# Kernel tuning notes

Measured on AMD Instinct MI355X. Metric: run time of the kernel, lower is better.

Reference implementation:

```python
import jax, jax.numpy as jnp
import numpy as np

N = 100000   # nodes
E = 1000000  # edges (avg degree 10)
F_IN, H1, H2, C = 128, 64, 64, 16


def setup_inputs() -> dict:
    key = jax.random.key(0)
    ks = jax.random.split(key, 10)
    x = jax.random.normal(ks[0], (N, F_IN), dtype=jnp.float32)
    edge_src = jax.random.randint(ks[1], (E,), 0, N, dtype=jnp.int32)
    edge_dst = jax.random.randint(ks[2], (E,), 0, N, dtype=jnp.int32)
    # normalized-adjacency-like positive edge weights (~1/deg scale)
    edge_val = jax.random.uniform(ks[3], (E,), dtype=jnp.float32) * 0.1
    def glorot(k, fan_in, fan_out):
        s = np.float32(1.0 / np.sqrt(fan_in))
        return jax.random.normal(k, (fan_in, fan_out), dtype=jnp.float32) * s
    W1 = glorot(ks[4], F_IN, H1)
    W2 = glorot(ks[5], H1, H2)
    W3 = glorot(ks[6], H2, C)
    b1 = jnp.zeros((H1,), jnp.float32)
    b2 = jnp.zeros((H2,), jnp.float32)
    b3 = jnp.zeros((C,), jnp.float32)
    return {"x": x, "edge_val": edge_val, "W1": W1, "b1": b1,
            "W2": W2, "b2": b2, "W3": W3, "b3": b3,
            "edge_src": edge_src, "edge_dst": edge_dst}


def gcn_layer(h, W, b, edge_src, edge_dst, edge_val):
    # support = h @ W ; out = spmm(adj, support) + b
    support = h @ W                                  # [N, d_out]
    msg = support[edge_src] * edge_val[:, None]      # [E, d_out] gather + scale
    agg = jax.ops.segment_sum(msg, edge_dst, num_segments=N)  # scatter-add
    return agg + b


def reference(x, edge_val, W1, b1, W2, b2, W3, b3, edge_src, edge_dst):
    # eval mode: F.dropout(training=False) is identity
    h = jax.nn.relu(gcn_layer(x, W1, b1, edge_src, edge_dst, edge_val))
    h = jax.nn.relu(gcn_layer(h, W2, b2, edge_src, edge_dst, edge_val))
    return gcn_layer(h, W3, b3, edge_src, edge_dst, edge_val)  # [N, C] logits
```

## Files before the change

### kernel.cpp

```cpp
#include <hip/hip_runtime.h>
#include <stdint.h>

#define N_NODES 100000
#define N_EDGES 1000000
#define NBUCK 98

typedef __attribute__((ext_vector_type(8))) __bf16 bf16x8;
typedef __attribute__((ext_vector_type(4))) float f32x4;

static __device__ __forceinline__ float bf2f(unsigned short u) {
    return __uint_as_float(((unsigned int)u) << 16);
}
static __device__ __forceinline__ unsigned short f2bf(float f) {
    unsigned int u = __float_as_uint(f);
    unsigned int r = (u + 0x7FFFu + ((u >> 16) & 1u)) >> 16;
    return (unsigned short)r;
}
static __device__ __forceinline__ float4 ld4_half(const unsigned short* p) {
    ushort4 u = *(const ushort4*)p;
    return make_float4(bf2f(u.x), bf2f(u.y), bf2f(u.z), bf2f(u.w));
}
static __device__ __forceinline__ void st4_half(unsigned short* p, float4 f) {
    ushort4 u;
    u.x = f2bf(f.x); u.y = f2bf(f.y); u.z = f2bf(f.z); u.w = f2bf(f.w);
    *(ushort4*)p = u;
}

static __device__ __forceinline__ float ldf(const void* p, size_t i, int bf) {
    return bf ? bf2f(((const unsigned short*)p)[i]) : ((const float*)p)[i];
}
static __device__ __forceinline__ float4 ldf4(const void* p, size_t i, int bf) {
    if (bf) return ld4_half((const unsigned short*)p + i);
    return *(const float4*)((const float*)p + i);
}

__global__ __launch_bounds__(256) void detect_kernel(const unsigned short* __restrict__ xs,
                                                     int* __restrict__ flag) {
    __shared__ int sz;
    if (threadIdx.x == 0) sz = 0;
    __syncthreads();
    int z = 0;
    for (int i = threadIdx.x; i < 1024; i += 256) {
        float av = fabsf(bf2f(xs[2 * i]));
        if (!(av <= 1048576.0f) || (av != 0.0f && av < 9.5367431640625e-07f)) z++;
    }
    atomicAdd(&sz, z);
    __syncthreads();
    if (threadIdx.x == 0) *flag = (sz > 256) ? 0 : 1;
}

__global__ __launch_bounds__(256) void bhist_kernel(const int* __restrict__ dst,
                                                    int* __restrict__ bcount) {
    __shared__ int cnt[NBUCK];
    int tid = threadIdx.x;
    for (int i = tid; i < NBUCK; i += 256) cnt[i] = 0;
    __syncthreads();
    int e0 = blockIdx.x * 4096;
#pragma unroll
    for (int i = 0; i < 16; ++i) {
        int e = e0 + i * 256 + tid;
        if (e < N_EDGES) atomicAdd(&cnt[dst[e] >> 10], 1);
    }
    __syncthreads();
    for (int i = tid; i < NBUCK; i += 256) {
        int c = cnt[i];
        if (c) atomicAdd(&bcount[i], c);
    }
}

__global__ __launch_bounds__(128) void bscan_kernel(const int* __restrict__ bcount,
                                                    int* __restrict__ bstart,
                                                    int* __restrict__ bcursor) {
    __shared__ int sh[128];
    int tid = threadIdx.x;
    int v = (tid < NBUCK) ? bcount[tid] : 0;
    sh[tid] = v;
    __syncthreads();
    for (int off = 1; off < 128; off <<= 1) {
        int t = 0;
        if (tid >= off) t = sh[tid - off];
        __syncthreads();
        if (tid >= off) sh[tid] += t;
        __syncthreads();
    }
    if (tid < NBUCK) {
        int excl = sh[tid] - v;
        bstart[tid] = excl;
        bcursor[tid] = excl;
    }
    if (tid == NBUCK - 1) bstart[NBUCK] = sh[tid];
}

__global__ __launch_bounds__(256) void part_kernel(const int* __restrict__ src,
                                                   const int* __restrict__ dst,
                                                   const void* __restrict__ val,
                                                   int* __restrict__ bcursor,
                                                   int2* __restrict__ part,
                                                   const int* __restrict__ flagp) {
    __shared__ int cnt[NBUCK];
    __shared__ int base[NBUCK];
    const int bf = *flagp;
    const int tid = threadIdx.x;
    const int e0 = blockIdx.x * 2048;
    for (int i = tid; i < NBUCK; i += 256) cnt[i] = 0;
    __syncthreads();
    int rank[8], bkt[8], pk[8], vb[8];
#pragma unroll
    for (int i = 0; i < 8; ++i) {
        int e = e0 + i * 256 + tid;
        bkt[i] = -1;
        if (e < N_EDGES) {
            int d = dst[e];
            int b = d >> 10;
            bkt[i] = b;
            pk[i] = src[e] | ((d & 1023) << 17);
            vb[i] = __float_as_int(ldf(val, e, bf));
            rank[i] = atomicAdd(&cnt[b], 1);
        }
    }
    __syncthreads();
    for (int i = tid; i < NBUCK; i += 256) {
        int c = cnt[i];
        base[i] = c ? atomicAdd(&bcursor[i], c) : 0;
    }
    __syncthreads();
#pragma unroll
    for (int i = 0; i < 8; ++i) {
        if (bkt[i] >= 0) part[(size_t)base[bkt[i]] + rank[i]] = make_int2(pk[i], vb[i]);
    }
}

__global__ __launch_bounds__(512) void place_kernel(const int* __restrict__ bstart,
                                                    const int2* __restrict__ part,
                                                    int* __restrict__ row_start,
                                                    int2* __restrict__ csr_rec) {
    __shared__ int cnt[1024];
    __shared__ int sums[512];
    const int tid = threadIdx.x;
    const int b = blockIdx.x;
    const int row0 = b << 10;
    const int nrows = min(1024, N_NODES - row0);
    const int s = bstart[b], e = bstart[b + 1];

    for (int i = tid; i < 1024; i += 512) cnt[i] = 0;
    __syncthreads();
    for (int j = s + tid; j < e; j += 512) {
        unsigned p = (unsigned)part[j].x;
        atomicAdd(&cnt[p >> 17], 1);
    }
    __syncthreads();
    int a0 = cnt[2 * tid], a1 = cnt[2 * tid + 1];
    int ts = a0 + a1;
    sums[tid] = ts;
    __syncthreads();
    for (int off = 1; off < 512; off <<= 1) {
        int t = 0;
        if (tid >= off) t = sums[tid - off];
        __syncthreads();
        if (tid >= off) sums[tid] += t;
        __syncthreads();
    }
    int excl = sums[tid] - ts;
    cnt[2 * tid] = s + excl;
    cnt[2 * tid + 1] = s + excl + a0;
    if (2 * tid < nrows)     row_start[row0 + 2 * tid] = s + excl;
    if (2 * tid + 1 < nrows) row_start[row0 + 2 * tid + 1] = s + excl + a0;
    if (b == NBUCK - 1 && tid == 0) row_start[N_NODES] = e;
    __syncthreads();
    for (int j = s + tid; j < e; j += 512) {
        int2 r = part[j];
        unsigned p = (unsigned)r.x;
        int pos = atomicAdd(&cnt[p >> 17], 1);
        csr_rec[pos] = make_int2((int)(p & 0x1FFFFu), r.y);
    }
}

template <int K, int M, bool DYNIN>
__global__ __launch_bounds__(256, 4) void mgemm_kernel(const void* __restrict__ hv_,
                                                       const void* __restrict__ W,
                                                       unsigned short* __restrict__ out,
                                                       const int* __restrict__ flagp) {
    constexpr int KP = K + 8;
    constexpr int NC = M / 16;
    constexpr int NK = K / 32;
    constexpr int NT = (N_NODES + 63) / 64;

    __shared__ unsigned short wt[M][KP];

    const int bf = *flagp;
    const int tid = threadIdx.x;

    for (int i = tid; i < K * M; i += 256) {
        int k = i / M, m = i % M;
        wt[m][k] = f2bf(ldf(W, i, bf));
    }
    __syncthreads();

    const int lane = tid & 63;
    const int qd = lane >> 4;
    const int ln = lane & 15;
    const int wrow = (tid >> 6) * 16;

    bf16x8 bfrag[NK][NC];
#pragma unroll
    for (int ks = 0; ks < NK; ++ks)
#pragma unroll
        for (int c = 0; c < NC; ++c)
            bfrag[ks][c] = *(const bf16x8*)&wt[c * 16 + ln][ks * 32 + qd * 8];

    for (int tile = blockIdx.x; tile < NT; tile += gridDim.x) {
        const int row = tile * 64 + wrow + ln;
        const bool ok = row < N_NODES;

        f32x4 acc[NC];
#pragma unroll
        for (int c = 0; c < NC; ++c) acc[c] = (f32x4){0.f, 0.f, 0.f, 0.f};

#pragma unroll
        for (int ks = 0; ks < NK; ++ks) {
            bf16x8 a;
            if (ok) {
                const size_t base = (size_t)row * K + ks * 32 + qd * 8;
                if (DYNIN && !bf) {
                    const float* xp = (const float*)hv_ + base;
                    float4 f0 = *(const float4*)xp;
                    float4 f1 = *(const float4*)(xp + 4);
                    ushort4 u0, u1;
                    u0.x = f2bf(f0.x); u0.y = f2bf(f0.y); u0.z = f2bf(f0.z); u0.w = f2bf(f0.w);
                    u1.x = f2bf(f1.x); u1.y = f2bf(f1.y); u1.z = f2bf(f1.z); u1.w = f2bf(f1.w);
                    ushort4 uu[2] = {u0, u1};
                    a = *(const bf16x8*)uu;
                } else {
                    a = *(const bf16x8*)((const unsigned short*)hv_ + base);
                }
            } else {
                a = (bf16x8)(__bf16)0.0f;
            }
#pragma unroll
            for (int c = 0; c < NC; ++c)
                acc[c] = __builtin_amdgcn_mfma_f32_16x16x32_bf16(a, bfrag[ks][c], acc[c], 0, 0, 0);
        }

#pragma unroll
        for (int c = 0; c < NC; ++c) {
#pragma unroll
            for (int r = 0; r < 4; ++r) {
                int orow = tile * 64 + wrow + qd * 4 + r;
                if (orow < N_NODES) out[(size_t)orow * M + c * 16 + ln] = f2bf(acc[c][r]);
            }
        }
    }
}

template <int M, bool RELU, bool DYNOUT>
__global__ __launch_bounds__(256) void spmm_kernel(const unsigned short* __restrict__ support,
                                                   const int* __restrict__ row_start,
                                                   const int2* __restrict__ csr_rec,
                                                   const void* __restrict__ bias,
                                                   void* __restrict__ out_,
                                                   const int* __restrict__ flagp) {
    constexpr int GROUP = M / 4;
    constexpr int GPB = 256 / GROUP;
    int bf = *flagp;
    int tid = threadIdx.x;
    int gid = blockIdx.x * GPB + tid / GROUP;
    int c0 = (tid % GROUP) * 4;
    if (gid >= N_NODES) return;
    int s = row_start[gid];
    int e = row_start[gid + 1];
    float a0 = ldf(bias, c0 + 0, bf);
    float a1 = ldf(bias, c0 + 1, bf);
    float a2 = ldf(bias, c0 + 2, bf);
    float a3 = ldf(bias, c0 + 3, bf);
    const unsigned short* supc = support + c0;

    int j = s;
    for (; j + 3 < e; j += 4) {
        int2 r0 = csr_rec[j + 0];
        int2 r1 = csr_rec[j + 1];
        int2 r2 = csr_rec[j + 2];
        int2 r3 = csr_rec[j + 3];
        float4 s0 = ld4_half(supc + (size_t)r0.x * M);
        float4 s1 = ld4_half(supc + (size_t)r1.x * M);
        float4 s2 = ld4_half(supc + (size_t)r2.x * M);
        float4 s3 = ld4_half(supc + (size_t)r3.x * M);
        float v0 = __int_as_float(r0.y);
        float v1 = __int_as_float(r1.y);
        float v2 = __int_as_float(r2.y);
        float v3 = __int_as_float(r3.y);
        a0 += v0 * s0.x; a1 += v0 * s0.y; a2 += v0 * s0.z; a3 += v0 * s0.w;
        a0 += v1 * s1.x; a1 += v1 * s1.y; a2 += v1 * s1.z; a3 += v1 * s1.w;
        a0 += v2 * s2.x; a1 += v2 * s2.y; a2 += v2 * s2.z; a3 += v2 * s2.w;
        a0 += v3 * s3.x; a1 += v3 * s3.y; a2 += v3 * s3.z; a3 += v3 * s3.w;
    }
    for (; j < e; ++j) {
        int2 rec = csr_rec[j];
        float v = __int_as_float(rec.y);
        float4 sp = ld4_half(supc + (size_t)rec.x * M);
        a0 += v * sp.x; a1 += v * sp.y; a2 += v * sp.z; a3 += v * sp.w;
    }
    if (RELU) {
        a0 = fmaxf(a0, 0.f); a1 = fmaxf(a1, 0.f);
        a2 = fmaxf(a2, 0.f); a3 = fmaxf(a3, 0.f);
    }
    float4 f = make_float4(a0, a1, a2, a3);
    if (DYNOUT) {
        if (bf) st4_half((unsigned short*)out_ + (size_t)gid * M + c0, f);
        else    *(float4*)((float*)out_ + (size_t)gid * M + c0) = f;
    } else {
        st4_half((unsigned short*)out_ + (size_t)gid * M + c0, f);
    }
}

extern "C" void kernel_launch(void* const* d_in, const int* in_sizes, int n_in,
                              void* d_out, int out_size, void* d_ws, size_t ws_size,
                              hipStream_t stream) {
    (void)in_sizes; (void)n_in; (void)out_size; (void)ws_size;
    const void* x  = d_in[0];
    const void* ev = d_in[1];
    const void* W1 = d_in[2];
    const void* b1 = d_in[3];
    const void* W2 = d_in[4];
    const void* b2 = d_in[5];
    const void* W3 = d_in[6];
    const void* b3 = d_in[7];
    const int* esrc = (const int*)d_in[8];
    const int* edst = (const int*)d_in[9];

    char* ws = (char*)d_ws;
    size_t off = 0;
    auto alloc = [&](size_t bytes) -> void* {
        void* p = ws + off;
        off = (off + bytes + 255) & ~(size_t)255;
        return p;
    };
    unsigned short* A = (unsigned short*)alloc((size_t)N_NODES * 64 * 2);
    unsigned short* B = (unsigned short*)alloc((size_t)N_NODES * 64 * 2);
    int* row_start  = (int*)alloc((size_t)(N_NODES + 1) * 4);
    int* bcount     = (int*)alloc(512);
    int* bstart     = (int*)alloc(512);
    int* bcursor    = (int*)alloc(512);
    int2* csr_rec   = (int2*)alloc((size_t)N_EDGES * 8);
    int* flagp      = (int*)alloc(256);
    int2* part      = (int2*)A;

    detect_kernel<<<1, 256, 0, stream>>>((const unsigned short*)x, flagp);

    hipMemsetAsync(bcount, 0, 512, stream);
    bhist_kernel<<<(N_EDGES + 4095) / 4096, 256, 0, stream>>>(edst, bcount);
    bscan_kernel<<<1, 128, 0, stream>>>(bcount, bstart, bcursor);
    part_kernel<<<(N_EDGES + 2047) / 2048, 256, 0, stream>>>(esrc, edst, ev, bcursor, part, flagp);
    place_kernel<<<NBUCK, 512, 0, stream>>>(bstart, part, row_start, csr_rec);

    int gm   = 1024;
    int gs64 = (N_NODES + 15) / 16;
    int g64  = (N_NODES + 63) / 64;

    mgemm_kernel<128, 64, true><<<gm, 256, 0, stream>>>(x, W1, A, flagp);
    spmm_kernel<64, true, false><<<gs64, 256, 0, stream>>>(A, row_start, csr_rec, b1, B, flagp);
    mgemm_kernel<64, 64, false><<<gm, 256, 0, stream>>>(B, W2, A, flagp);
    spmm_kernel<64, true, false><<<gs64, 256, 0, stream>>>(A, row_start, csr_rec, b2, B, flagp);
    mgemm_kernel<64, 16, false><<<gm, 256, 0, stream>>>(B, W3, A, flagp);
    spmm_kernel<16, false, true><<<g64, 256, 0, stream>>>(A, row_start, csr_rec, b3, d_out, flagp);
}
```

Measured before the change: 277.3 us.

## Fuse SpMM aggregation with following GEMM via shared-memory tile

The 64-wide SpMM+ReLU of layers 1 and 2 is merged with the next layer's dense matmul: each block gathers a 64-row tile into LDS as bf16, then runs MFMA against the next weight matrix. This drops two kernel launches and a round trip of the intermediate activations through global memory. The gather loop is also unrolled to 8 edges to keep more loads in flight. The first GEMM now reads weight fragments from LDS inside the loop instead of keeping them in registers. The fused kernel uses a persistent grid of 1024 blocks with barriers per tile, so fewer concurrent row gathers may hide less latency than the old per-row spmm grid.

```diff
diff --git a/kernel.cpp b/kernel.cpp
--- a/kernel.cpp
+++ b/kernel.cpp
@@ -175,6 +175,46 @@
     }
 }
 
+static __device__ __forceinline__ void row_gather(const unsigned short* __restrict__ supc,
+                                                  const int2* __restrict__ csr_rec,
+                                                  int s, int e, int M,
+                                                  float& a0, float& a1, float& a2, float& a3) {
+    int j = s;
+    for (; j + 7 < e; j += 8) {
+        int2 r[8];
+#pragma unroll
+        for (int t = 0; t < 8; ++t) r[t] = csr_rec[j + t];
+        float4 sp[8];
+#pragma unroll
+        for (int t = 0; t < 8; ++t) sp[t] = ld4_half(supc + (size_t)r[t].x * M);
+#pragma unroll
+        for (int t = 0; t < 8; ++t) {
+            float v = __int_as_float(r[t].y);
+            a0 += v * sp[t].x; a1 += v * sp[t].y; a2 += v * sp[t].z; a3 += v * sp[t].w;
+        }
+    }
+    if (j + 3 < e) {
+        int2 r[4];
+#pragma unroll
+        for (int t = 0; t < 4; ++t) r[t] = csr_rec[j + t];
+        float4 sp[4];
+#pragma unroll
+        for (int t = 0; t < 4; ++t) sp[t] = ld4_half(supc + (size_t)r[t].x * M);
+#pragma unroll
+        for (int t = 0; t < 4; ++t) {
+            float v = __int_as_float(r[t].y);
+            a0 += v * sp[t].x; a1 += v * sp[t].y; a2 += v * sp[t].z; a3 += v * sp[t].w;
+        }
+        j += 4;
+    }
+    for (; j < e; ++j) {
+        int2 rec = csr_rec[j];
+        float v = __int_as_float(rec.y);
+        float4 sp = ld4_half(supc + (size_t)rec.x * M);
+        a0 += v * sp.x; a1 += v * sp.y; a2 += v * sp.z; a3 += v * sp.w;
+    }
+}
+
 template <int K, int M, bool DYNIN>
 __global__ __launch_bounds__(256, 4) void mgemm_kernel(const void* __restrict__ hv_,
                                                        const void* __restrict__ W,
@@ -201,13 +241,6 @@
     const int ln = lane & 15;
     const int wrow = (tid >> 6) * 16;
 
-    bf16x8 bfrag[NK][NC];
-#pragma unroll
-    for (int ks = 0; ks < NK; ++ks)
-#pragma unroll
-        for (int c = 0; c < NC; ++c)
-            bfrag[ks][c] = *(const bf16x8*)&wt[c * 16 + ln][ks * 32 + qd * 8];
-
     for (int tile = blockIdx.x; tile < NT; tile += gridDim.x) {
         const int row = tile * 64 + wrow + ln;
         const bool ok = row < N_NODES;
@@ -225,10 +258,9 @@
                     const float* xp = (const float*)hv_ + base;
                     float4 f0 = *(const float4*)xp;
                     float4 f1 = *(const float4*)(xp + 4);
-                    ushort4 u0, u1;
-                    u0.x = f2bf(f0.x); u0.y = f2bf(f0.y); u0.z = f2bf(f0.z); u0.w = f2bf(f0.w);
-                    u1.x = f2bf(f1.x); u1.y = f2bf(f1.y); u1.z = f2bf(f1.z); u1.w = f2bf(f1.w);
-                    ushort4 uu[2] = {u0, u1};
+                    ushort4 uu[2];
+                    uu[0].x = f2bf(f0.x); uu[0].y = f2bf(f0.y); uu[0].z = f2bf(f0.z); uu[0].w = f2bf(f0.w);
+                    uu[1].x = f2bf(f1.x); uu[1].y = f2bf(f1.y); uu[1].z = f2bf(f1.z); uu[1].w = f2bf(f1.w);
                     a = *(const bf16x8*)uu;
                 } else {
                     a = *(const bf16x8*)((const unsigned short*)hv_ + base);
@@ -237,8 +269,10 @@
                 a = (bf16x8)(__bf16)0.0f;
             }
 #pragma unroll
-            for (int c = 0; c < NC; ++c)
-                acc[c] = __builtin_amdgcn_mfma_f32_16x16x32_bf16(a, bfrag[ks][c], acc[c], 0, 0, 0);
+            for (int c = 0; c < NC; ++c) {
+                bf16x8 b = *(const bf16x8*)&wt[c * 16 + ln][ks * 32 + qd * 8];
+                acc[c] = __builtin_amdgcn_mfma_f32_16x16x32_bf16(a, b, acc[c], 0, 0, 0);
+            }
         }
 
 #pragma unroll
@@ -252,19 +286,105 @@
     }
 }
 
-template <int M, bool RELU, bool DYNOUT>
-__global__ __launch_bounds__(256) void spmm_kernel(const unsigned short* __restrict__ support,
-                                                   const int* __restrict__ row_start,
-                                                   const int2* __restrict__ csr_rec,
-                                                   const void* __restrict__ bias,
-                                                   void* __restrict__ out_,
-                                                   const int* __restrict__ flagp) {
-    constexpr int GROUP = M / 4;
-    constexpr int GPB = 256 / GROUP;
+template <int MOUT>
+__global__ __launch_bounds__(256, 4) void fused_kernel(const unsigned short* __restrict__ support,
+                                                       const int* __restrict__ row_start,
+                                                       const int2* __restrict__ csr_rec,
+                                                       const void* __restrict__ bias,
+                                                       const void* __restrict__ W,
+                                                       unsigned short* __restrict__ out,
+                                                       const int* __restrict__ flagp) {
+    constexpr int K = 64, KP = 72;
+    constexpr int NC = MOUT / 16;
+    constexpr int NK = 2;
+    constexpr int NT = (N_NODES + 63) / 64;
+
+    __shared__ unsigned short agg[64][KP];
+    __shared__ unsigned short wt[MOUT][KP];
+
+    const int bf = *flagp;
+    const int tid = threadIdx.x;
+
+    for (int i = tid; i < K * MOUT; i += 256) {
+        int k = i / MOUT, m = i % MOUT;
+        wt[m][k] = f2bf(ldf(W, i, bf));
+    }
+    __syncthreads();
+
+    const int lane = tid & 63;
+    const int qd = lane >> 4;
+    const int ln = lane & 15;
+    const int wrow = (tid >> 6) * 16;
+
+    bf16x8 bfrag[NK][NC];
+#pragma unroll
+    for (int ks = 0; ks < NK; ++ks)
+#pragma unroll
+        for (int c = 0; c < NC; ++c)
+            bfrag[ks][c] = *(const bf16x8*)&wt[c * 16 + ln][ks * 32 + qd * 8];
+
+    const int grp = tid >> 4;
+    const int cc = tid & 15;
+    const float bs0 = ldf(bias, cc * 4 + 0, bf);
+    const float bs1 = ldf(bias, cc * 4 + 1, bf);
+    const float bs2 = ldf(bias, cc * 4 + 2, bf);
+    const float bs3 = ldf(bias, cc * 4 + 3, bf);
+    const unsigned short* supc = support + cc * 4;
+
+    for (int tile = blockIdx.x; tile < NT; tile += gridDim.x) {
+#pragma unroll
+        for (int rr = 0; rr < 4; ++rr) {
+            int rl = grp * 4 + rr;
+            int row = tile * 64 + rl;
+            float a0 = bs0, a1 = bs1, a2 = bs2, a3 = bs3;
+            if (row < N_NODES) {
+                int s = row_start[row];
+                int e = row_start[row + 1];
+                row_gather(supc, csr_rec, s, e, 64, a0, a1, a2, a3);
+                a0 = fmaxf(a0, 0.f); a1 = fmaxf(a1, 0.f);
+                a2 = fmaxf(a2, 0.f); a3 = fmaxf(a3, 0.f);
+            } else {
+                a0 = a1 = a2 = a3 = 0.f;
+            }
+            st4_half(&agg[rl][cc * 4], make_float4(a0, a1, a2, a3));
+        }
+        __syncthreads();
+
+        f32x4 acc[NC];
+#pragma unroll
+        for (int c = 0; c < NC; ++c) acc[c] = (f32x4){0.f, 0.f, 0.f, 0.f};
+#pragma unroll
+        for (int ks = 0; ks < NK; ++ks) {
+            bf16x8 a = *(const bf16x8*)&agg[wrow + ln][ks * 32 + qd * 8];
+#pragma unroll
+            for (int c = 0; c < NC; ++c)
+                acc[c] = __builtin_amdgcn_mfma_f32_16x16x32_bf16(a, bfrag[ks][c], acc[c], 0, 0, 0);
+        }
+
+#pragma unroll
+        for (int c = 0; c < NC; ++c) {
+#pragma unroll
+            for (int r = 0; r < 4; ++r) {
+                int orow = tile * 64 + wrow + qd * 4 + r;
+                if (orow < N_NODES) out[(size_t)orow * MOUT + c * 16 + ln] = f2bf(acc[c][r]);
+            }
+        }
+        __syncthreads();
+    }
+}
+
+template <bool DYNOUT>
+__global__ __launch_bounds__(256) void spmm16_kernel(const unsigned short* __restrict__ support,
+                                                     const int* __restrict__ row_start,
+                                                     const int2* __restrict__ csr_rec,
+                                                     const void* __restrict__ bias,
+                                                     void* __restrict__ out_,
+                                                     const int* __restrict__ flagp) {
+    constexpr int M = 16;
     int bf = *flagp;
     int tid = threadIdx.x;
-    int gid = blockIdx.x * GPB + tid / GROUP;
-    int c0 = (tid % GROUP) * 4;
+    int gid = blockIdx.x * 64 + tid / 4;
+    int c0 = (tid % 4) * 4;
     if (gid >= N_NODES) return;
     int s = row_start[gid];
     int e = row_start[gid + 1];
@@ -272,44 +392,10 @@
     float a1 = ldf(bias, c0 + 1, bf);
     float a2 = ldf(bias, c0 + 2, bf);
     float a3 = ldf(bias, c0 + 3, bf);
-    const unsigned short* supc = support + c0;
-
-    int j = s;
-    for (; j + 3 < e; j += 4) {
-        int2 r0 = csr_rec[j + 0];
-        int2 r1 = csr_rec[j + 1];
-        int2 r2 = csr_rec[j + 2];
-        int2 r3 = csr_rec[j + 3];
-        float4 s0 = ld4_half(supc + (size_t)r0.x * M);
-        float4 s1 = ld4_half(supc + (size_t)r1.x * M);
-        float4 s2 = ld4_half(supc + (size_t)r2.x * M);
-        float4 s3 = ld4_half(supc + (size_t)r3.x * M);
-        float v0 = __int_as_float(r0.y);
-        float v1 = __int_as_float(r1.y);
-        float v2 = __int_as_float(r2.y);
-        float v3 = __int_as_float(r3.y);
-        a0 += v0 * s0.x; a1 += v0 * s0.y; a2 += v0 * s0.z; a3 += v0 * s0.w;
-        a0 += v1 * s1.x; a1 += v1 * s1.y; a2 += v1 * s1.z; a3 += v1 * s1.w;
-        a0 += v2 * s2.x; a1 += v2 * s2.y; a2 += v2 * s2.z; a3 += v2 * s2.w;
-        a0 += v3 * s3.x; a1 += v3 * s3.y; a2 += v3 * s3.z; a3 += v3 * s3.w;
-    }
-    for (; j < e; ++j) {
-        int2 rec = csr_rec[j];
-        float v = __int_as_float(rec.y);
-        float4 sp = ld4_half(supc + (size_t)rec.x * M);
-        a0 += v * sp.x; a1 += v * sp.y; a2 += v * sp.z; a3 += v * sp.w;
-    }
-    if (RELU) {
-        a0 = fmaxf(a0, 0.f); a1 = fmaxf(a1, 0.f);
-        a2 = fmaxf(a2, 0.f); a3 = fmaxf(a3, 0.f);
-    }
+    row_gather(support + c0, csr_rec, s, e, M, a0, a1, a2, a3);
     float4 f = make_float4(a0, a1, a2, a3);
-    if (DYNOUT) {
-        if (bf) st4_half((unsigned short*)out_ + (size_t)gid * M + c0, f);
-        else    *(float4*)((float*)out_ + (size_t)gid * M + c0) = f;
-    } else {
-        st4_half((unsigned short*)out_ + (size_t)gid * M + c0, f);
-    }
+    if (DYNOUT && !bf) *(float4*)((float*)out_ + (size_t)gid * M + c0) = f;
+    else               st4_half((unsigned short*)out_ + (size_t)gid * M + c0, f);
 }
 
 extern "C" void kernel_launch(void* const* d_in, const int* in_sizes, int n_in,
@@ -352,14 +438,8 @@
     part_kernel<<<(N_EDGES + 2047) / 2048, 256, 0, stream>>>(esrc, edst, ev, bcursor, part, flagp);
     place_kernel<<<NBUCK, 512, 0, stream>>>(bstart, part, row_start, csr_rec);
 
-    int gm   = 1024;
-    int gs64 = (N_NODES + 15) / 16;
-    int g64  = (N_NODES + 63) / 64;
-
-    mgemm_kernel<128, 64, true><<<gm, 256, 0, stream>>>(x, W1, A, flagp);
-    spmm_kernel<64, true, false><<<gs64, 256, 0, stream>>>(A, row_start, csr_rec, b1, B, flagp);
-    mgemm_kernel<64, 64, false><<<gm, 256, 0, stream>>>(B, W2, A, flagp);
-    spmm_kernel<64, true, false><<<gs64, 256, 0, stream>>>(A, row_start, csr_rec, b2, B, flagp);
-    mgemm_kernel<64, 16, false><<<gm, 256, 0, stream>>>(B, W3, A, flagp);
-    spmm_kernel<16, false, true><<<g64, 256, 0, stream>>>(A, row_start, csr_rec, b3, d_out, flagp);
-}
+    mgemm_kernel<128, 64, true><<<1024, 256, 0, stream>>>(x, W1, A, flagp);
+    fused_kernel<64><<<1024, 256, 0, stream>>>(A, row_start, csr_rec, b1, W2, B, flagp);
+    fused_kernel<16><<<1024, 256, 0, stream>>>(B, row_start, csr_rec, b2, W3, A, flagp);
+    spmm16_kernel<true><<<(N_NODES + 63) / 64, 256, 0, stream>>>(A, row_start, csr_rec, b3, d_out, flagp);
+}
```

Result: faster. 266.0 us (-4.1%).
